# Kernel tuning notes

Measured on AMD Instinct MI355X. Metric: run time of the kernel, lower is better.

## Reference

```python
import jax, jax.numpy as jnp
import numpy as np

N_HEADS = 16
EMB_DIM = 1024
HEAD_DIM = EMB_DIM // N_HEADS


def setup_inputs() -> dict:
    key = jax.random.key(0)
    k1, k2, k3, k4, k5 = jax.random.split(key, 5)
    s = 1.0 / np.sqrt(EMB_DIM)
    return {
        "attn_in": jax.random.normal(k1, (4, 2048, EMB_DIM), dtype=jnp.float32),
        "W_qkv": jax.random.uniform(k2, (EMB_DIM, 3 * EMB_DIM), jnp.float32, -s, s),
        "b_qkv": jax.random.uniform(k3, (3 * EMB_DIM,), jnp.float32, -s, s),
        "W_out": jax.random.uniform(k4, (EMB_DIM, EMB_DIM), jnp.float32, -s, s),
        "b_out": jax.random.uniform(k5, (EMB_DIM,), jnp.float32, -s, s),
    }


def reference(attn_in, W_qkv, b_qkv, W_out, b_out):
    N, L, E = attn_in.shape
    qkv = attn_in @ W_qkv + b_qkv                      # [N, L, 3E]
    q, k, v = jnp.split(qkv, 3, axis=-1)
    # [N, L, E] -> [N, H, L, D]
    def heads(x):
        return x.reshape(N, L, N_HEADS, HEAD_DIM).transpose(0, 2, 1, 3)
    q, k, v = heads(q), heads(k), heads(v)
    scale = 1.0 / np.sqrt(HEAD_DIM)
    scores = jnp.einsum('nhqd,nhkd->nhqk', q, k) * scale   # [N, H, L, L]
    attn = jax.nn.softmax(scores, axis=-1)
    o = jnp.einsum('nhqk,nhkd->nhqd', attn, v)             # [N, H, L, D]
    o = o.transpose(0, 2, 1, 3).reshape(N, L, E)
    return o @ W_out + b_out
```

## Files before the change

kernel.cpp:

```cpp
#include <hip/hip_runtime.h>

typedef __attribute__((ext_vector_type(8))) short short8;
typedef __attribute__((ext_vector_type(4))) float f32x4;
typedef __attribute__((ext_vector_type(16))) float f32x16;

#define MFMA16(A,B,C) __builtin_amdgcn_mfma_f32_16x16x32_bf16(A,B,C,0,0,0)
#define MFMA32(A,B,C) __builtin_amdgcn_mfma_f32_32x32x16_bf16(A,B,C,0,0,0)

__device__ __forceinline__ short f2bf(float f){
  union { float f; unsigned int u; } v; v.f = f;
  unsigned int u = v.u;
  unsigned int r = (u + 0x7fffu + ((u >> 16) & 1u)) >> 16;
  return (short)r;
}

__device__ __forceinline__ unsigned pk2bf_hu(float x, float y){
  unsigned a = __builtin_bit_cast(unsigned, x) + 0x8000u;
  unsigned b = __builtin_bit_cast(unsigned, y) + 0x8000u;
  return __builtin_amdgcn_perm(b, a, 0x07060302u);
}

typedef const __attribute__((address_space(1))) void* gptr_t;
typedef __attribute__((address_space(3))) void* lptr_t;

__device__ __forceinline__ void gload16(const short* g, short* l){
  __builtin_amdgcn_global_load_lds((gptr_t)g, (lptr_t)l, 16, 0, 0);
}


__global__ __launch_bounds__(256) void cvt_x_kernel(const float* __restrict__ x,
                                                    short* __restrict__ xb){
  const size_t i = (size_t)blockIdx.x * 256 + threadIdx.x;
  const float4* p = (const float4*)x + i * 2;
  float4 a = p[0], b = p[1];
  short8 o;
  o[0]=f2bf(a.x); o[1]=f2bf(a.y); o[2]=f2bf(a.z); o[3]=f2bf(a.w);
  o[4]=f2bf(b.x); o[5]=f2bf(b.y); o[6]=f2bf(b.z); o[7]=f2bf(b.w);
  *(short8*)(xb + i * 8) = o;
}

__global__ __launch_bounds__(256) void cvt_t_kernel(const float* __restrict__ src,
                                                    short* __restrict__ dst,
                                                    int R, int C){
  __shared__ float tile[32][33];
  const int tx = threadIdx.x, ty = threadIdx.y;
  const int c0 = blockIdx.x * 32, r0 = blockIdx.y * 32;
  #pragma unroll
  for (int i = 0; i < 32; i += 8)
    tile[ty + i][tx] = src[(size_t)(r0 + ty + i) * C + c0 + tx];
  __syncthreads();
  #pragma unroll
  for (int i = 0; i < 32; i += 8)
    dst[(size_t)(c0 + ty + i) * R + r0 + tx] = f2bf(tile[tx][ty + i]);
}


template<int EPI>
__global__ __launch_bounds__(256) void gemm_bt(
    const short* __restrict__ A, const short* __restrict__ BT,
    const float* __restrict__ bias,
    float* __restrict__ Cf,
    short* __restrict__ q_ws, short* __restrict__ k_ws, short* __restrict__ vt_ws)
{
  __shared__ __align__(16) short As[4096];
  __shared__ __align__(16) short Bs[4096];
  const int tid = threadIdx.x;
  const int bm = blockIdx.x, bn = blockIdx.y;
  const int lane = tid & 63, wid = tid >> 6;
  const int wr = wid >> 1, wc = wid & 1;
  const int r = lane & 15, g = lane >> 4;

  f32x4 acc[4][4] = {};

  const short* ag = A  + (size_t)(bm * 128 + (tid >> 2)) * 1024 + (tid & 3) * 8;
  const short* bg = BT + (size_t)(bn * 128 + (tid >> 2)) * 1024 + (tid & 3) * 8;
  short* asd = &As[tid * 8];
  short* bsd = &Bs[tid * 8];

  for (int kk = 0; kk < 32; ++kk){
    gload16(ag + kk * 32,             asd);
    gload16(ag + kk * 32 + 64 * 1024, asd + 2048);
    gload16(bg + kk * 32,             bsd);
    gload16(bg + kk * 32 + 64 * 1024, bsd + 2048);
    asm volatile("s_waitcnt vmcnt(0)" ::: "memory");
    __syncthreads();
    short8 a[4], b[4];
    #pragma unroll
    for (int mf = 0; mf < 4; ++mf)
      a[mf] = *(const short8*)&As[(wr * 64 + mf * 16 + r) * 32 + g * 8];
    #pragma unroll
    for (int nf = 0; nf < 4; ++nf)
      b[nf] = *(const short8*)&Bs[(wc * 64 + nf * 16 + r) * 32 + g * 8];
    #pragma unroll
    for (int mf = 0; mf < 4; ++mf)
      #pragma unroll
      for (int nf = 0; nf < 4; ++nf)
        acc[mf][nf] = MFMA16(a[mf], b[nf], acc[mf][nf]);
    __syncthreads();
  }

  if (EPI == 0){
    #pragma unroll
    for (int nf = 0; nf < 4; ++nf){
      const int c = bn * 128 + wc * 64 + nf * 16 + r;
      const float bv = bias[c];
      const int type = c >> 10;
      const int h = (c & 1023) >> 6, d = c & 63;
      const float mul = (type == 0) ? 0.18033688011112042f : 1.0f;
      #pragma unroll
      for (int mf = 0; mf < 4; ++mf){
        const int row0 = bm * 128 + wr * 64 + mf * 16 + g * 4;
        const int nb = row0 >> 11, l0 = row0 & 2047;
        f32x4 v = acc[mf][nf];
        if (type == 2){
          short4 pk;
          pk.x = f2bf(v[0] + bv); pk.y = f2bf(v[1] + bv);
          pk.z = f2bf(v[2] + bv); pk.w = f2bf(v[3] + bv);
          const int head = nb * 16 + h;
          *(short4*)&vt_ws[(((size_t)head * 32 + (l0 >> 6)) * 64 + d) * 64 + (l0 & 63)] = pk;
        } else {
          short* dst = (type == 0) ? q_ws : k_ws;
          const size_t base = ((size_t)(nb * 16 + h) * 2048 + l0) * 64 + d;
          #pragma unroll
          for (int j = 0; j < 4; ++j)
            dst[base + (size_t)j * 64] = f2bf((v[j] + bv) * mul);
        }
      }
    }
  } else {
    #pragma unroll
    for (int nf = 0; nf < 4; ++nf){
      const int c = bn * 128 + wc * 64 + nf * 16 + r;
      const float bv = bias[c];
      #pragma unroll
      for (int mf = 0; mf < 4; ++mf){
        const int row0 = bm * 128 + wr * 64 + mf * 16 + g * 4;
        f32x4 v = acc[mf][nf];
        #pragma unroll
        for (int j = 0; j < 4; ++j)
          Cf[(size_t)(row0 + j) * 1024 + c] = v[j] + bv;
      }
    }
  }
}


__global__ __launch_bounds__(512, 4) void attn_kernel(
    const short* __restrict__ qw, const short* __restrict__ kw,
    const short* __restrict__ vtw, short* __restrict__ ow)
{
  __shared__ __align__(16) short Ks[4][4096];
  __shared__ __align__(16) short Vs[4][4096];

  const int id = blockIdx.x;
  const int xcd = id & 7, j2 = id >> 3;
  const int nh = xcd * 8 + (j2 & 7);
  const int qt = j2 >> 3;
  const int tid = threadIdx.x;
  const int lane = tid & 63, w = tid >> 6;
  const int l31 = lane & 31, hi = lane >> 5, w7 = lane & 7;

  const size_t hoff = (size_t)nh * 2048 * 64;
  const short* kh = kw + hoff;
  const short* vh = vtw + hoff;

  const int srow = tid >> 3, schunk = tid & 7;
  const int scw = (schunk ^ (srow & 7)) * 8;
  const short* ksrc = kh + srow * 64 + scw;
  const short* vsrc = vh + srow * 64 + scw;

  unsigned aoffh[2][4];
  #pragma unroll
  for (int T = 0; T < 2; ++T)
    #pragma unroll
    for (int s = 0; s < 4; ++s)
      aoffh[T][s] = (unsigned)((l31 + 32 * T) * 64 + (((2 * s + hi) ^ w7) * 8));

  const int qrow0 = qt * 256 + w * 32;
  short8 qfr[4];
  #pragma unroll
  for (int s = 0; s < 4; ++s)
    qfr[s] = *(const short8*)(qw + hoff + (size_t)(qrow0 + l31) * 64 + s * 16 + hi * 8);

  f32x16 oa0 = {}, oa1 = {}, lacc = {};
  short8 onesB;
  #pragma unroll
  for (int i = 0; i < 8; ++i) onesB[i] = (short)0x3F80;

  auto compute = [&](const short* Kb, const short* Vb){
    f32x16 ss0, ss1;
    {
      const f32x16 zz = {};
      ss0 = MFMA32(*(const short8*)&Kb[aoffh[0][0]], qfr[0], zz);
      ss1 = MFMA32(*(const short8*)&Kb[aoffh[1][0]], qfr[0], zz);
    }
    #pragma unroll
    for (int s = 1; s < 4; ++s){
      ss0 = MFMA32(*(const short8*)&Kb[aoffh[0][s]], qfr[s], ss0);
      ss1 = MFMA32(*(const short8*)&Kb[aoffh[1][s]], qfr[s], ss1);
    }

    unsigned u0[8], u1[8];
    #pragma unroll
    for (int m = 0; m < 8; ++m){
      u0[m] = pk2bf_hu(__builtin_amdgcn_exp2f(ss0[2 * m]),
                       __builtin_amdgcn_exp2f(ss0[2 * m + 1]));
      u1[m] = pk2bf_hu(__builtin_amdgcn_exp2f(ss1[2 * m]),
                       __builtin_amdgcn_exp2f(ss1[2 * m + 1]));
    }

    short8 pa[4];
    #pragma unroll
    for (int s = 0; s < 4; ++s){
      const int sg = (s & 1) * 4;
      unsigned a0 = (s < 2) ? u0[sg + 0] : u1[sg + 0];
      unsigned a1 = (s < 2) ? u0[sg + 1] : u1[sg + 1];
      unsigned a2 = (s < 2) ? u0[sg + 2] : u1[sg + 2];
      unsigned a3 = (s < 2) ? u0[sg + 3] : u1[sg + 3];
      auto r02 = __builtin_amdgcn_permlane32_swap(a0, a2, false, false);
      auto r13 = __builtin_amdgcn_permlane32_swap(a1, a3, false, false);
      union { unsigned q[4]; short8 s8; } cv;
      cv.q[0] = (unsigned)r02[0]; cv.q[1] = (unsigned)r13[0];
      cv.q[2] = (unsigned)r02[1]; cv.q[3] = (unsigned)r13[1];
      pa[s] = cv.s8;
    }

    #pragma unroll
    for (int s = 0; s < 4; ++s){
      oa0  = MFMA32(pa[s], *(const short8*)&Vb[aoffh[0][s]], oa0);
      oa1  = MFMA32(pa[s], *(const short8*)&Vb[aoffh[1][s]], oa1);
      lacc = MFMA32(pa[s], onesB, lacc);
    }
  };

  gload16(ksrc,        &Ks[0][tid * 8]);
  gload16(vsrc,        &Vs[0][tid * 8]);
  gload16(ksrc + 4096, &Ks[1][tid * 8]);
  gload16(vsrc + 4096, &Vs[1][tid * 8]);

  for (int p = 0; p < 8; ++p){
    const int t0 = p * 4;
    asm volatile("s_waitcnt vmcnt(0)" ::: "memory");
    asm volatile("s_barrier" ::: "memory");
    gload16(ksrc + (t0 + 2) * 4096, &Ks[2][tid * 8]);
    gload16(vsrc + (t0 + 2) * 4096, &Vs[2][tid * 8]);
    gload16(ksrc + (t0 + 3) * 4096, &Ks[3][tid * 8]);
    gload16(vsrc + (t0 + 3) * 4096, &Vs[3][tid * 8]);
    compute(&Ks[0][0], &Vs[0][0]);
    compute(&Ks[1][0], &Vs[1][0]);
    asm volatile("s_waitcnt vmcnt(0)" ::: "memory");
    asm volatile("s_barrier" ::: "memory");
    {
      const int ts0 = (t0 + 4) & 31;
      const int ts1 = (t0 + 5) & 31;
      gload16(ksrc + ts0 * 4096, &Ks[0][tid * 8]);
      gload16(vsrc + ts0 * 4096, &Vs[0][tid * 8]);
      gload16(ksrc + ts1 * 4096, &Ks[1][tid * 8]);
      gload16(vsrc + ts1 * 4096, &Vs[1][tid * 8]);
    }
    compute(&Ks[2][0], &Vs[2][0]);
    compute(&Ks[3][0], &Vs[3][0]);
  }

  const int n = nh >> 4, h = nh & 15;
  #pragma unroll
  for (int j = 0; j < 16; ++j){
    const float inv = 1.0f / lacc[j];
    const int qr = (j & 3) + 8 * (j >> 2) + 4 * hi;
    const size_t base = ((size_t)n * 2048 + qrow0 + qr) * 1024 + h * 64 + l31;
    ow[base]      = f2bf(oa0[j] * inv);
    ow[base + 32] = f2bf(oa1[j] * inv);
  }
}


extern "C" void kernel_launch(void* const* d_in, const int* in_sizes, int n_in,
                              void* d_out, int out_size, void* d_ws, size_t ws_size,
                              hipStream_t stream){
  const float* attn_in = (const float*)d_in[0];
  const float* W_qkv   = (const float*)d_in[1];
  const float* b_qkv   = (const float*)d_in[2];
  const float* W_out   = (const float*)d_in[3];
  const float* b_out   = (const float*)d_in[4];
  float* out = (float*)d_out;

  char* ws = (char*)d_ws;
  short* xb    = (short*)(ws);
  short* wqT   = (short*)(ws + 16777216);
  short* woT   = (short*)(ws + 23068672);
  short* q_ws  = (short*)(ws + 25165824);
  short* k_ws  = (short*)(ws + 41943040);
  short* vt_ws = (short*)(ws + 58720256);
  short* o_ws  = (short*)(ws + 75497472);

  cvt_x_kernel<<<4096, 256, 0, stream>>>(attn_in, xb);
  cvt_t_kernel<<<dim3(96, 32), dim3(32, 8), 0, stream>>>(W_qkv, wqT, 1024, 3072);
  cvt_t_kernel<<<dim3(32, 32), dim3(32, 8), 0, stream>>>(W_out, woT, 1024, 1024);
  gemm_bt<0><<<dim3(64, 24), 256, 0, stream>>>(xb, wqT, b_qkv, nullptr, q_ws, k_ws, vt_ws);
  attn_kernel<<<512, 512, 0, stream>>>(q_ws, k_ws, vt_ws, o_ws);
  gemm_bt<1><<<dim3(64, 8), 256, 0, stream>>>(o_ws, woT, b_out, out, nullptr, nullptr, nullptr);
}
```

Before: 191.3 us.

## Quad-buffer GEMM LDS tiles to overlap global loads with MFMA compute

```diff
diff --git a/kernel.cpp b/kernel.cpp
--- a/kernel.cpp
+++ b/kernel.cpp
@@ -62,8 +62,8 @@
     float* __restrict__ Cf,
     short* __restrict__ q_ws, short* __restrict__ k_ws, short* __restrict__ vt_ws)
 {
-  __shared__ __align__(16) short As[4096];
-  __shared__ __align__(16) short Bs[4096];
+  __shared__ __align__(16) short As[4][4096];
+  __shared__ __align__(16) short Bs[4][4096];
   const int tid = threadIdx.x;
   const int bm = blockIdx.x, bn = blockIdx.y;
   const int lane = tid & 63, wid = tid >> 6;
@@ -74,29 +74,46 @@
 
   const short* ag = A  + (size_t)(bm * 128 + (tid >> 2)) * 1024 + (tid & 3) * 8;
   const short* bg = BT + (size_t)(bn * 128 + (tid >> 2)) * 1024 + (tid & 3) * 8;
-  short* asd = &As[tid * 8];
-  short* bsd = &Bs[tid * 8];
-
-  for (int kk = 0; kk < 32; ++kk){
-    gload16(ag + kk * 32,             asd);
-    gload16(ag + kk * 32 + 64 * 1024, asd + 2048);
-    gload16(bg + kk * 32,             bsd);
-    gload16(bg + kk * 32 + 64 * 1024, bsd + 2048);
-    asm volatile("s_waitcnt vmcnt(0)" ::: "memory");
-    __syncthreads();
-    short8 a[4], b[4];
+
+  auto stage = [&](int kk, int b){
+    gload16(ag + kk * 32,             &As[b][tid * 8]);
+    gload16(ag + kk * 32 + 64 * 1024, &As[b][tid * 8 + 2048]);
+    gload16(bg + kk * 32,             &Bs[b][tid * 8]);
+    gload16(bg + kk * 32 + 64 * 1024, &Bs[b][tid * 8 + 2048]);
+  };
+
+  auto compute = [&](int b){
+    short8 a[4], bb[4];
     #pragma unroll
     for (int mf = 0; mf < 4; ++mf)
-      a[mf] = *(const short8*)&As[(wr * 64 + mf * 16 + r) * 32 + g * 8];
+      a[mf] = *(const short8*)&As[b][(wr * 64 + mf * 16 + r) * 32 + g * 8];
     #pragma unroll
     for (int nf = 0; nf < 4; ++nf)
-      b[nf] = *(const short8*)&Bs[(wc * 64 + nf * 16 + r) * 32 + g * 8];
+      bb[nf] = *(const short8*)&Bs[b][(wc * 64 + nf * 16 + r) * 32 + g * 8];
     #pragma unroll
     for (int mf = 0; mf < 4; ++mf)
       #pragma unroll
       for (int nf = 0; nf < 4; ++nf)
-        acc[mf][nf] = MFMA16(a[mf], b[nf], acc[mf][nf]);
-    __syncthreads();
+        acc[mf][nf] = MFMA16(a[mf], bb[nf], acc[mf][nf]);
+  };
+
+  stage(0, 0);
+  stage(1, 1);
+
+  for (int p = 0; p < 8; ++p){
+    const int t0 = p * 4;
+    asm volatile("s_waitcnt vmcnt(0)" ::: "memory");
+    asm volatile("s_barrier" ::: "memory");
+    stage(t0 + 2, 2);
+    stage(t0 + 3, 3);
+    compute(0);
+    compute(1);
+    asm volatile("s_waitcnt vmcnt(0)" ::: "memory");
+    asm volatile("s_barrier" ::: "memory");
+    stage((t0 + 4) & 31, 0);
+    stage((t0 + 5) & 31, 1);
+    compute(2);
+    compute(3);
   }
 
   if (EPI == 0){
```

Result: slower. 235.4 us (+23.0%).
